# Kernel tuning notes

Hardware: AMD Instinct MI355X
Metric: run time of the kernel (lower is better)

## Reference

```python
import jax, jax.numpy as jnp
import numpy as np

B, D0, D1 = 4096, 128, 128
T, DEPTH, W = 64, 2, 4          # num_tree, depth, width
S = W ** (DEPTH + 1)            # num_state = 64
NODES = sum(W ** l for l in range(DEPTH + 1))  # 21 internal nodes per tree
D = D0 + D1


def setup_inputs() -> dict:
    key = jax.random.key(0)
    ks = jax.random.split(key, 9)
    inp0 = jax.random.normal(ks[0], (B, D0), jnp.float32)
    inp1 = jax.random.normal(ks[1], (B, D1), jnp.float32)
    x2 = jax.random.normal(ks[2], (B,), jnp.float32)
    # ForestLinear: per-tree, per-node linear maps to `width` branch logits
    W_nodes = 0.02 * jax.random.normal(ks[3], (T, NODES, D, W), jnp.float32)
    b_nodes = jnp.zeros((T, NODES, W), jnp.float32)
    # MultiDense([0,1], 1): per-(tree,state) linear probe per input
    W0 = 0.02 * jax.random.normal(ks[4], (T, S, D0), jnp.float32)
    b0 = jnp.zeros((T, S), jnp.float32)
    W1 = 0.02 * jax.random.normal(ks[5], (T, S, D1), jnp.float32)
    b1 = jnp.zeros((T, S), jnp.float32)
    return {"inp0": inp0, "inp1": inp1, "x2": x2,
            "W_nodes": W_nodes, "b_nodes": b_nodes,
            "W0": W0, "b0": b0, "W1": W1, "b1": b1}


def _forest_states(x, W_nodes, b_nodes):
    # x: [B, D] -> leaf-state probabilities [B, T, S]
    logits = jnp.einsum('bd,tndw->btnw', x, W_nodes) + b_nodes  # [B,T,NODES,W]
    probs = jax.nn.softmax(logits, axis=-1)
    p = jnp.ones((x.shape[0], T, 1), probs.dtype)
    off = 0
    for l in range(DEPTH + 1):
        n = W ** l
        pl = probs[:, :, off:off + n, :]                 # [B,T,n,W]
        p = (p[..., None] * pl).reshape(x.shape[0], T, n * W)
        off += n
    return p  # [B, T, S]


def reference(inp0, inp1, x2, W_nodes, b_nodes, W0, b0, W1, b1):
    x_states = _forest_states(jnp.concatenate([inp0, inp1], axis=-1), W_nodes, b_nodes)
    # per-tree/state linear probes; equivalent to tile + MultiDense, no materialized tile
    x_pred = (jnp.einsum('bd,tsd->bts', inp0, W0) + b0
              + jnp.einsum('bd,tsd->bts', inp1, W1) + b1)  # [B,T,S]
    y_pred_logit_parallel = x2[:, None, None] + x_pred
    ave_pred_tree = jnp.sum(x_states * jax.nn.sigmoid(y_pred_logit_parallel), axis=2)  # [B,T]
    ave_pred = jnp.mean(ave_pred_tree, axis=1)  # [B]
    return (y_pred_logit_parallel, ave_pred)
```

## Files before the change

kernel.cpp:

```cpp
#include <hip/hip_runtime.h>

#define B_SZ    4096
#define DD      256
#define T_TREES 64
#define NNODES  21
#define S_LEAF  64
#define M_TILE  128
#define HBYTES  40960
#define WBYTES  (2 * HBYTES)
#define XOFF    ((size_t)T_TREES * WBYTES)
#define QBYTES  20480


typedef __attribute__((ext_vector_type(8))) short  short8;
typedef __attribute__((ext_vector_type(4))) float  f32x4;

#define DPP_ADD(x, ctrl) ((x) + __int_as_float(__builtin_amdgcn_mov_dpp(__float_as_int(x), (ctrl), 0xF, 0xF, true)))
#define DPP_MOV(x, ctrl) __int_as_float(__builtin_amdgcn_mov_dpp(__float_as_int(x), (ctrl), 0xF, 0xF, true))
__device__ __forceinline__ float qsum4(float x) {
    x = DPP_ADD(x, 0xB1);
    x = DPP_ADD(x, 0x4E);
    return x;
}
__device__ __forceinline__ float rsum16(float x) {
    x = DPP_ADD(x, 0xB1);
    x = DPP_ADD(x, 0x4E);
    x = DPP_ADD(x, 0x124);
    x = DPP_ADD(x, 0x128);
    return x;
}

__device__ __forceinline__ unsigned short f2bf(float f) {
    unsigned int u = __float_as_uint(f);
    u += 0x7fffu + ((u >> 16) & 1u);
    return (unsigned short)(u >> 16);
}
__device__ __forceinline__ void gl2lds16(const void* g, void* l) {
    __builtin_amdgcn_global_load_lds(
        (const __attribute__((address_space(1))) unsigned int*)g,
        (__attribute__((address_space(3))) unsigned int*)l, 16, 0, 0);
}
__device__ __host__ __forceinline__ int woffh(int c, int klo) {
    return c * 256 + (((klo ^ c) & 15) << 4);
}
__device__ __host__ __forceinline__ int woffq(int c, int klo) {
    return (c >> 1) * 256 + (((((klo << 1) ^ (c & 14))) | (c & 1)) << 4);
}

__global__ void zero_ave_kernel(float* __restrict__ out1) {
    int i = blockIdx.x * 256 + threadIdx.x;
    if (i < B_SZ) out1[i] = 0.0f;
}

__global__ void prep_weights(const float* __restrict__ Wn, const float* __restrict__ W0,
                             const float* __restrict__ W1, const float* __restrict__ inp0,
                             const float* __restrict__ inp1, char* __restrict__ ws,
                             float* __restrict__ out1) {
    int id = blockIdx.x * 256 + threadIdx.x;
    if (id < 43008) {
        int oct  = id & 31;
        int rest = id >> 5;
        int n    = rest % NNODES;
        int t    = rest / NNODES;
        int h    = oct >> 4, klo = oct & 15;
        const f32x4* src = (const f32x4*)(Wn + (((size_t)t * NNODES + n) * DD + oct * 8) * 4);
        f32x4 v[8];
        #pragma unroll
        for (int j = 0; j < 8; ++j) v[j] = src[j];
        char* base = ws + (size_t)t * WBYTES + h * HBYTES;
        #pragma unroll
        for (int w = 0; w < 4; ++w) {
            int c = n * 4 + w + (n >= 5 ? 12 : 0);
            short8 pack;
            #pragma unroll
            for (int j = 0; j < 8; ++j) pack[j] = (short)f2bf(v[j][w]);
            *(short8*)(base + woffh(c, klo)) = pack;
        }
    } else if (id < 67584) {
        int idx  = id - 43008;
        int kc   = idx & 31;
        int rest = idx >> 5;
        int c    = 20 + rest % 12;
        int t    = rest / 12;
        short8 z = (short8){0,0,0,0,0,0,0,0};
        *(short8*)(ws + (size_t)t * WBYTES + (kc >> 4) * HBYTES + woffh(c, kc & 15)) = z;
    } else if (id < 198656) {
        int idx = id - 67584;
        int kc  = idx & 31;
        int s   = (idx >> 5) & 63;
        int t   = idx >> 11;
        int k0  = kc * 8;
        const float* src = (k0 < 128) ? (W0 + ((size_t)t * S_LEAF + s) * 128 + k0)
                                      : (W1 + ((size_t)t * S_LEAF + s) * 128 + (k0 - 128));
        short8 pack;
        #pragma unroll
        for (int j = 0; j < 8; ++j) pack[j] = (short)f2bf(src[j]);
        *(short8*)(ws + (size_t)t * WBYTES + (kc >> 4) * HBYTES + woffh(96 + s, kc & 15)) = pack;
    } else if (id < 202752) {
        out1[id - 198656] = 0.0f;
    } else if (id < 333824) {
        int idx = id - 202752;
        int oct = idx & 31;
        int r   = idx >> 5;
        const float* src = (oct < 16) ? (inp0 + (size_t)r * 128 + oct * 8)
                                      : (inp1 + (size_t)r * 128 + (oct - 16) * 8);
        f32x4 f0 = *(const f32x4*)src;
        f32x4 f1 = *(const f32x4*)(src + 4);
        short8 pack;
        pack[0]=(short)f2bf(f0[0]); pack[1]=(short)f2bf(f0[1]);
        pack[2]=(short)f2bf(f0[2]); pack[3]=(short)f2bf(f0[3]);
        pack[4]=(short)f2bf(f1[0]); pack[5]=(short)f2bf(f1[1]);
        pack[6]=(short)f2bf(f1[2]); pack[7]=(short)f2bf(f1[3]);
        *(short8*)(ws + XOFF + ((size_t)r * DD + oct * 8) * 2) = pack;
    }
}

__global__ __launch_bounds__(256, 3)
void forest_main(const float* __restrict__ x2,  const float* __restrict__ bn,
                 const float* __restrict__ b0,  const float* __restrict__ b1,
                 const char* __restrict__ wsW,
                 float* __restrict__ out0, float* __restrict__ out1) {
    __shared__ __align__(16) char smem[HBYTES];

    const int tid  = threadIdx.x;
    const int orig = blockIdx.x;
    const int swz  = (orig & 7) * 256 + (orig >> 3);
    const int t    = swz >> 5;
    const int mt   = swz & 31;
    const int m0   = mt * M_TILE;
    const int lane = tid & 63;
    const int wid  = tid >> 6;
    const int ri   = lane & 15;
    const int kg   = lane >> 4;

    const unsigned short* xbf = (const unsigned short*)(wsW + XOFF);
    const char* wbase = wsW + (size_t)t * WBYTES;

    f32x4 acc[2][10];
    #pragma unroll
    for (int sr = 0; sr < 2; ++sr)
        #pragma unroll
        for (int ct = 0; ct < 10; ++ct)
            acc[sr][ct] = (f32x4){0.f, 0.f, 0.f, 0.f};

    const int gr0r = m0 + wid * 32 + ri;
    const int gr1r = gr0r + 16;

    for (int h = 0; h < 2; ++h) {
        {
            const char* src = wbase + h * HBYTES + tid * 16;
            char* dst = smem + tid * 16;
            #pragma unroll
            for (int it = 0; it < 10; ++it)
                gl2lds16(src + it * 4096, dst + it * 4096);
        }
        __syncthreads();

        #pragma unroll
        for (int ks = 0; ks < 4; ++ks) {
            const int kk = h * 4 + ks;
            short8 a0 = *(const short8*)(xbf + (size_t)gr0r * DD + kk * 32 + kg * 8);
            short8 a1 = *(const short8*)(xbf + (size_t)gr1r * DD + kk * 32 + kg * 8);
            const int klo = ks * 4 + kg;
            const int dsB = ri * 256 + (((klo ^ ri) & 15) << 4);
            #pragma unroll
            for (int ct = 0; ct < 10; ++ct) {
                short8 bv = *(const short8*)(smem + dsB + ct * 4096);
                acc[0][ct] = __builtin_amdgcn_mfma_f32_16x16x32_bf16(a0, bv, acc[0][ct], 0, 0, 0);
                acc[1][ct] = __builtin_amdgcn_mfma_f32_16x16x32_bf16(a1, bv, acc[1][ct], 0, 0, 0);
            }
        }
        if (h == 0) __syncthreads();
    }

    const int kgbase = kg * 16;
    #pragma unroll
    for (int sr = 0; sr < 2; ++sr) {
        const int rlBase = wid * 32 + sr * 16 + kg * 4;
        const int gr0 = m0 + rlBase;
        f32x4 x2v = *(const f32x4*)(x2 + gr0);
        float bn0 = bn[t * 84 + ri];
        float bn1 = bn[t * 84 + 16 + (ri & 3)];

        float L1r[4];
        #pragma unroll
        for (int r = 0; r < 4; ++r) {
            float e0 = __expf(acc[sr][0][r] + bn0);
            float p0 = e0 * __builtin_amdgcn_rcpf(qsum4(e0));
            float e1 = __expf(acc[sr][1][r] + bn1);
            float p1 = e1 * __builtin_amdgcn_rcpf(qsum4(e1));
            float pa  = __shfl(p0, kgbase + (ri >> 2));
            float pb0 = DPP_MOV(p0, 0x124);
            float pb1 = DPP_MOV(p1, 0x124);
            L1r[r] = pa * ((ri < 12) ? pb0 : pb1);
        }
        float partial[4] = {0.f, 0.f, 0.f, 0.f};
        #pragma unroll
        for (int ct = 0; ct < 4; ++ct) {
            int s = ct * 16 + ri;
            float bn2 = bn[t * 84 + 20 + s];
            float bb  = b0[t * S_LEAF + s] + b1[t * S_LEAF + s];
            #pragma unroll
            for (int r = 0; r < 4; ++r) {
                float e = __expf(acc[sr][2 + ct][r] + bn2);
                float p2 = e * __builtin_amdgcn_rcpf(qsum4(e));
                float L2 = p2 * __shfl(L1r[r], kgbase + ct * 4 + (ri >> 2));
                float y = acc[sr][6 + ct][r] + x2v[r] + bb;
                out0[((size_t)(gr0 + r) * T_TREES + t) * S_LEAF + s] = y;
                float sg = __builtin_amdgcn_rcpf(1.0f + __expf(-y));
                partial[r] += sg * L2;
            }
        }
        #pragma unroll
        for (int r = 0; r < 4; ++r) {
            float p = rsum16(partial[r]);
            if (ri == 0) atomicAdd(out1 + gr0 + r, p * (1.0f / T_TREES));
        }
    }
}

__device__ __forceinline__ short8 ldAraw(const float* __restrict__ inp0,
                                         const float* __restrict__ inp1,
                                         int gr, int kkidx, int kg) {
    int k0 = kkidx * 32 + kg * 8;
    const float* src = (k0 < 128) ? (inp0 + (size_t)gr * 128 + k0)
                                  : (inp1 + (size_t)gr * 128 + (k0 - 128));
    f32x4 f0 = *(const f32x4*)src;
    f32x4 f1 = *(const f32x4*)(src + 4);
    short8 a;
    a[0]=(short)f2bf(f0[0]); a[1]=(short)f2bf(f0[1]);
    a[2]=(short)f2bf(f0[2]); a[3]=(short)f2bf(f0[3]);
    a[4]=(short)f2bf(f1[0]); a[5]=(short)f2bf(f1[1]);
    a[6]=(short)f2bf(f1[2]); a[7]=(short)f2bf(f1[3]);
    return a;
}

__global__ __launch_bounds__(256, 2)
void forest_fb(const float* __restrict__ inp0, const float* __restrict__ inp1,
               const float* __restrict__ x2,   const float* __restrict__ Wn,
               const float* __restrict__ bn,   const float* __restrict__ W0,
               const float* __restrict__ b0,   const float* __restrict__ W1,
               const float* __restrict__ b1,
               float* __restrict__ out0, float* __restrict__ out1) {
    __shared__ __align__(16) char smem[QBYTES];

    const int tid  = threadIdx.x;
    const int orig = blockIdx.x;
    const int swz  = (orig & 7) * 256 + (orig >> 3);
    const int t    = swz >> 5;
    const int mt   = swz & 31;
    const int m0   = mt * 128;
    const int lane = tid & 63;
    const int wid  = tid >> 6;
    const int ri   = lane & 15;
    const int kg   = lane >> 4;

    f32x4 acc[2][10];
    #pragma unroll
    for (int sr = 0; sr < 2; ++sr)
        #pragma unroll
        for (int ct = 0; ct < 10; ++ct)
            acc[sr][ct] = (f32x4){0.f, 0.f, 0.f, 0.f};

    const int gr0r = m0 + wid * 32 + ri;
    const int gr1r = gr0r + 16;

    int dsb[2];
    #pragma unroll
    for (int kkl = 0; kkl < 2; ++kkl) {
        int klo = kkl * 4 + kg;
        dsb[kkl] = (ri >> 1) * 256 + (((((klo << 1) ^ (ri & 14))) | (ri & 1)) << 4);
    }

    for (int q = 0; q < 4; ++q) {
        #pragma unroll
        for (int it = 0; it < 5; ++it) {
            int idx = tid + it * 256;
            int c   = idx >> 3;
            int klo = idx & 7;
            int k0  = (q * 8 + klo) * 8;
            unsigned short v[8];
            if (c < 20) {
                int n = c >> 2, w = c & 3;
                const float* src = Wn + (((size_t)t * NNODES + n) * DD + k0) * 4 + w;
                #pragma unroll
                for (int j = 0; j < 8; ++j) v[j] = f2bf(src[j * 4]);
            } else if (c < 32) {
                #pragma unroll
                for (int j = 0; j < 8; ++j) v[j] = 0;
            } else if (c < 96) {
                int n = 5 + ((c - 32) >> 2), w = (c - 32) & 3;
                const float* src = Wn + (((size_t)t * NNODES + n) * DD + k0) * 4 + w;
                #pragma unroll
                for (int j = 0; j < 8; ++j) v[j] = f2bf(src[j * 4]);
            } else {
                int s = c - 96;
                const float* src = (k0 < 128) ? (W0 + ((size_t)t * S_LEAF + s) * 128 + k0)
                                              : (W1 + ((size_t)t * S_LEAF + s) * 128 + (k0 - 128));
                #pragma unroll
                for (int j = 0; j < 8; ++j) v[j] = f2bf(src[j]);
            }
            short8 pack;
            #pragma unroll
            for (int j = 0; j < 8; ++j) pack[j] = (short)v[j];
            *(short8*)(smem + woffq(c, klo)) = pack;
        }
        short8 a00 = ldAraw(inp0, inp1, gr0r, 2*q+0, kg);
        short8 a10 = ldAraw(inp0, inp1, gr1r, 2*q+0, kg);
        short8 a01 = ldAraw(inp0, inp1, gr0r, 2*q+1, kg);
        short8 a11 = ldAraw(inp0, inp1, gr1r, 2*q+1, kg);
        __syncthreads();
        #pragma unroll
        for (int ct = 0; ct < 10; ++ct) {
            short8 b0f = *(const short8*)(smem + dsb[0] + ct * 2048);
            acc[0][ct] = __builtin_amdgcn_mfma_f32_16x16x32_bf16(a00, b0f, acc[0][ct], 0, 0, 0);
            acc[1][ct] = __builtin_amdgcn_mfma_f32_16x16x32_bf16(a10, b0f, acc[1][ct], 0, 0, 0);
        }
        #pragma unroll
        for (int ct = 0; ct < 10; ++ct) {
            short8 b1f = *(const short8*)(smem + dsb[1] + ct * 2048);
            acc[0][ct] = __builtin_amdgcn_mfma_f32_16x16x32_bf16(a01, b1f, acc[0][ct], 0, 0, 0);
            acc[1][ct] = __builtin_amdgcn_mfma_f32_16x16x32_bf16(a11, b1f, acc[1][ct], 0, 0, 0);
        }
        if (q < 3) __syncthreads();
    }

    const int kgbase = kg * 16;
    #pragma unroll
    for (int sr = 0; sr < 2; ++sr) {
        const int rlBase = wid * 32 + sr * 16 + kg * 4;
        const int gr0 = m0 + rlBase;
        f32x4 x2v = *(const f32x4*)(x2 + gr0);
        float bn0 = bn[t * 84 + ri];
        float bn1 = bn[t * 84 + 16 + (ri & 3)];
        float L1r[4];
        #pragma unroll
        for (int r = 0; r < 4; ++r) {
            float e0 = __expf(acc[sr][0][r] + bn0);
            float p0 = e0 * __builtin_amdgcn_rcpf(qsum4(e0));
            float e1 = __expf(acc[sr][1][r] + bn1);
            float p1 = e1 * __builtin_amdgcn_rcpf(qsum4(e1));
            float pa  = __shfl(p0, kgbase + (ri >> 2));
            float pb0 = DPP_MOV(p0, 0x124);
            float pb1 = DPP_MOV(p1, 0x124);
            L1r[r] = pa * ((ri < 12) ? pb0 : pb1);
        }
        float partial[4] = {0.f, 0.f, 0.f, 0.f};
        #pragma unroll
        for (int ct = 0; ct < 4; ++ct) {
            int s = ct * 16 + ri;
            float bn2 = bn[t * 84 + 20 + s];
            float bb  = b0[t * S_LEAF + s] + b1[t * S_LEAF + s];
            #pragma unroll
            for (int r = 0; r < 4; ++r) {
                float e = __expf(acc[sr][2 + ct][r] + bn2);
                float p2 = e * __builtin_amdgcn_rcpf(qsum4(e));
                float L2 = p2 * __shfl(L1r[r], kgbase + ct * 4 + (ri >> 2));
                float y = acc[sr][6 + ct][r] + x2v[r] + bb;
                out0[((size_t)(gr0 + r) * T_TREES + t) * S_LEAF + s] = y;
                float sg = __builtin_amdgcn_rcpf(1.0f + __expf(-y));
                partial[r] += sg * L2;
            }
        }
        #pragma unroll
        for (int r = 0; r < 4; ++r) {
            float p = rsum16(partial[r]);
            if (ri == 0) atomicAdd(out1 + gr0 + r, p * (1.0f / T_TREES));
        }
    }
}

extern "C" void kernel_launch(void* const* d_in, const int* in_sizes, int n_in,
                              void* d_out, int out_size, void* d_ws, size_t ws_size,
                              hipStream_t stream) {
    const float* inp0 = (const float*)d_in[0];
    const float* inp1 = (const float*)d_in[1];
    const float* x2   = (const float*)d_in[2];
    const float* Wn   = (const float*)d_in[3];
    const float* bn   = (const float*)d_in[4];
    const float* W0   = (const float*)d_in[5];
    const float* b0   = (const float*)d_in[6];
    const float* W1   = (const float*)d_in[7];
    const float* b1   = (const float*)d_in[8];

    float* out0 = (float*)d_out;
    float* out1 = out0 + (size_t)B_SZ * T_TREES * S_LEAF;

    const size_t need = XOFF + (size_t)B_SZ * DD * 2;
    dim3 grid((B_SZ / M_TILE) * T_TREES);

    if (ws_size >= need) {
        hipLaunchKernelGGL(prep_weights, dim3(1304), dim3(256), 0, stream,
                           Wn, W0, W1, inp0, inp1, (char*)d_ws, out1);
        hipLaunchKernelGGL(forest_main, grid, dim3(256), 0, stream,
                           x2, bn, b0, b1, (const char*)d_ws, out0, out1);
    } else {
        hipLaunchKernelGGL(zero_ave_kernel, dim3((B_SZ + 255) / 256), dim3(256), 0, stream, out1);
        hipLaunchKernelGGL(forest_fb, grid, dim3(256), 0, stream,
                           inp0, inp1, x2, Wn, bn, W0, b0, W1, b1, out0, out1);
    }
}
```

Before: 52.99 us.

## Halve row tile and split column tiles across wave pairs with LDS handoff

Reduces the M tile from 128 to 64 rows, doubling the grid, and splits the 10 output column tiles between two wave groups (5 each), so each wave holds half the accumulators. The tree-probability epilogue is split as well: one wave group computes softmax path probabilities into an LDS table, and the other writes the logits, then combines them with sigmoid after a barrier. Lower register use allows a higher launch-bounds occupancy of 4, at the cost of loading each weight slab twice as often overall, plus an extra barrier and LDS traffic.

Result: slower. 65.57 us (+23.8%).

```diff
diff --git a/kernel.cpp b/kernel.cpp
--- a/kernel.cpp
+++ b/kernel.cpp
@@ -5,7 +5,7 @@
 #define T_TREES 64
 #define NNODES  21
 #define S_LEAF  64
-#define M_TILE  128
+#define M_TILE  64
 #define HBYTES  40960
 #define WBYTES  (2 * HBYTES)
 #define XOFF    ((size_t)T_TREES * WBYTES)
@@ -115,7 +115,7 @@
     }
 }
 
-__global__ __launch_bounds__(256, 3)
+__global__ __launch_bounds__(256, 4)
 void forest_main(const float* __restrict__ x2,  const float* __restrict__ bn,
                  const float* __restrict__ b0,  const float* __restrict__ b1,
                  const char* __restrict__ wsW,
@@ -124,26 +124,28 @@
 
     const int tid  = threadIdx.x;
     const int orig = blockIdx.x;
-    const int swz  = (orig & 7) * 256 + (orig >> 3);
-    const int t    = swz >> 5;
-    const int mt   = swz & 31;
+    const int swz  = (orig & 7) * 512 + (orig >> 3);
+    const int t    = swz >> 6;
+    const int mt   = swz & 63;
     const int m0   = mt * M_TILE;
     const int lane = tid & 63;
     const int wid  = tid >> 6;
+    const int wv   = wid & 1;
+    const int wr   = wid >> 1;
     const int ri   = lane & 15;
     const int kg   = lane >> 4;
 
     const unsigned short* xbf = (const unsigned short*)(wsW + XOFF);
     const char* wbase = wsW + (size_t)t * WBYTES;
 
-    f32x4 acc[2][10];
+    f32x4 acc[2][5];
     #pragma unroll
     for (int sr = 0; sr < 2; ++sr)
         #pragma unroll
-        for (int ct = 0; ct < 10; ++ct)
+        for (int ct = 0; ct < 5; ++ct)
             acc[sr][ct] = (f32x4){0.f, 0.f, 0.f, 0.f};
 
-    const int gr0r = m0 + wid * 32 + ri;
+    const int gr0r = m0 + wr * 32 + ri;
     const int gr1r = gr0r + 16;
 
     for (int h = 0; h < 2; ++h) {
@@ -162,59 +164,110 @@
             short8 a0 = *(const short8*)(xbf + (size_t)gr0r * DD + kk * 32 + kg * 8);
             short8 a1 = *(const short8*)(xbf + (size_t)gr1r * DD + kk * 32 + kg * 8);
             const int klo = ks * 4 + kg;
-            const int dsB = ri * 256 + (((klo ^ ri) & 15) << 4);
-            #pragma unroll
-            for (int ct = 0; ct < 10; ++ct) {
+            const int dsB = wv * 20480 + ri * 256 + (((klo ^ ri) & 15) << 4);
+            #pragma unroll
+            for (int ct = 0; ct < 5; ++ct) {
                 short8 bv = *(const short8*)(smem + dsB + ct * 4096);
                 acc[0][ct] = __builtin_amdgcn_mfma_f32_16x16x32_bf16(a0, bv, acc[0][ct], 0, 0, 0);
                 acc[1][ct] = __builtin_amdgcn_mfma_f32_16x16x32_bf16(a1, bv, acc[1][ct], 0, 0, 0);
             }
         }
-        if (h == 0) __syncthreads();
-    }
-
+        __syncthreads();
+    }
+
+    float* Ltab = (float*)smem;
+    float* L1s  = (float*)smem + 64 * 65;
     const int kgbase = kg * 16;
-    #pragma unroll
-    for (int sr = 0; sr < 2; ++sr) {
-        const int rlBase = wid * 32 + sr * 16 + kg * 4;
-        const int gr0 = m0 + rlBase;
-        f32x4 x2v = *(const f32x4*)(x2 + gr0);
-        float bn0 = bn[t * 84 + ri];
-        float bn1 = bn[t * 84 + 16 + (ri & 3)];
-
-        float L1r[4];
-        #pragma unroll
-        for (int r = 0; r < 4; ++r) {
-            float e0 = __expf(acc[sr][0][r] + bn0);
-            float p0 = e0 * __builtin_amdgcn_rcpf(qsum4(e0));
-            float e1 = __expf(acc[sr][1][r] + bn1);
-            float p1 = e1 * __builtin_amdgcn_rcpf(qsum4(e1));
-            float pa  = __shfl(p0, kgbase + (ri >> 2));
-            float pb0 = DPP_MOV(p0, 0x124);
-            float pb1 = DPP_MOV(p1, 0x124);
-            L1r[r] = pa * ((ri < 12) ? pb0 : pb1);
-        }
-        float partial[4] = {0.f, 0.f, 0.f, 0.f};
-        #pragma unroll
-        for (int ct = 0; ct < 4; ++ct) {
-            int s = ct * 16 + ri;
-            float bn2 = bn[t * 84 + 20 + s];
-            float bb  = b0[t * S_LEAF + s] + b1[t * S_LEAF + s];
+
+    float p48[2][4];
+
+    if (wv == 0) {
+        #pragma unroll
+        for (int sr = 0; sr < 2; ++sr) {
+            const int rowb = wr * 32 + sr * 16 + kg * 4;
+            float bn0 = bn[t * 84 + ri];
+            float bn1 = bn[t * 84 + 16 + (ri & 3)];
+            float L1r[4];
             #pragma unroll
             for (int r = 0; r < 4; ++r) {
-                float e = __expf(acc[sr][2 + ct][r] + bn2);
-                float p2 = e * __builtin_amdgcn_rcpf(qsum4(e));
-                float L2 = p2 * __shfl(L1r[r], kgbase + ct * 4 + (ri >> 2));
-                float y = acc[sr][6 + ct][r] + x2v[r] + bb;
-                out0[((size_t)(gr0 + r) * T_TREES + t) * S_LEAF + s] = y;
-                float sg = __builtin_amdgcn_rcpf(1.0f + __expf(-y));
-                partial[r] += sg * L2;
-            }
-        }
-        #pragma unroll
-        for (int r = 0; r < 4; ++r) {
-            float p = rsum16(partial[r]);
-            if (ri == 0) atomicAdd(out1 + gr0 + r, p * (1.0f / T_TREES));
+                float e0 = __expf(acc[sr][0][r] + bn0);
+                float p0 = e0 * __builtin_amdgcn_rcpf(qsum4(e0));
+                float e1 = __expf(acc[sr][1][r] + bn1);
+                float p1 = e1 * __builtin_amdgcn_rcpf(qsum4(e1));
+                float pa  = __shfl(p0, kgbase + (ri >> 2));
+                float pb0 = DPP_MOV(p0, 0x124);
+                float pb1 = DPP_MOV(p1, 0x124);
+                L1r[r] = pa * ((ri < 12) ? pb0 : pb1);
+                if (ri >= 12) L1s[(rowb + r) * 4 + (ri - 12)] = L1r[r];
+            }
+            #pragma unroll
+            for (int ct = 2; ct < 5; ++ct) {
+                int s = (ct - 2) * 16 + ri;
+                float bn2 = bn[t * 84 + 20 + s];
+                #pragma unroll
+                for (int r = 0; r < 4; ++r) {
+                    float e = __expf(acc[sr][ct][r] + bn2);
+                    float p2 = e * __builtin_amdgcn_rcpf(qsum4(e));
+                    float L2 = p2 * __shfl(L1r[r], kgbase + (ct - 2) * 4 + (ri >> 2));
+                    Ltab[(rowb + r) * 65 + s] = L2;
+                }
+            }
+        }
+    } else {
+        float bn2 = bn[t * 84 + 68 + ri];
+        #pragma unroll
+        for (int sr = 0; sr < 2; ++sr)
+            #pragma unroll
+            for (int r = 0; r < 4; ++r) {
+                float e = __expf(acc[sr][0][r] + bn2);
+                p48[sr][r] = e * __builtin_amdgcn_rcpf(qsum4(e));
+            }
+        #pragma unroll
+        for (int sr = 0; sr < 2; ++sr) {
+            const int gr0 = m0 + wr * 32 + sr * 16 + kg * 4;
+            f32x4 x2v = *(const f32x4*)(x2 + gr0);
+            #pragma unroll
+            for (int ct = 1; ct < 5; ++ct) {
+                int s = (ct - 1) * 16 + ri;
+                float bb = b0[t * S_LEAF + s] + b1[t * S_LEAF + s];
+                #pragma unroll
+                for (int r = 0; r < 4; ++r) {
+                    float y = acc[sr][ct][r] + x2v[r] + bb;
+                    out0[((size_t)(gr0 + r) * T_TREES + t) * S_LEAF + s] = y;
+                }
+            }
+        }
+    }
+    __syncthreads();
+
+    if (wv == 1) {
+        #pragma unroll
+        for (int sr = 0; sr < 2; ++sr) {
+            const int rowb = wr * 32 + sr * 16 + kg * 4;
+            const int gr0 = m0 + rowb;
+            f32x4 x2v = *(const f32x4*)(x2 + gr0);
+            float L2_48[4];
+            #pragma unroll
+            for (int r = 0; r < 4; ++r)
+                L2_48[r] = p48[sr][r] * L1s[(rowb + r) * 4 + (ri >> 2)];
+            float partial[4] = {0.f, 0.f, 0.f, 0.f};
+            #pragma unroll
+            for (int ct = 1; ct < 5; ++ct) {
+                int s = (ct - 1) * 16 + ri;
+                float bb = b0[t * S_LEAF + s] + b1[t * S_LEAF + s];
+                #pragma unroll
+                for (int r = 0; r < 4; ++r) {
+                    float y = acc[sr][ct][r] + x2v[r] + bb;
+                    float sg = __builtin_amdgcn_rcpf(1.0f + __expf(-y));
+                    float L2 = (ct < 4) ? Ltab[(rowb + r) * 65 + s] : L2_48[r];
+                    partial[r] += sg * L2;
+                }
+            }
+            #pragma unroll
+            for (int r = 0; r < 4; ++r) {
+                float p = rsum16(partial[r]);
+                if (ri == 0) atomicAdd(out1 + gr0 + r, p * (1.0f / T_TREES));
+            }
         }
     }
 }
@@ -387,16 +440,15 @@
     float* out1 = out0 + (size_t)B_SZ * T_TREES * S_LEAF;
 
     const size_t need = XOFF + (size_t)B_SZ * DD * 2;
-    dim3 grid((B_SZ / M_TILE) * T_TREES);
 
     if (ws_size >= need) {
         hipLaunchKernelGGL(prep_weights, dim3(1304), dim3(256), 0, stream,
                            Wn, W0, W1, inp0, inp1, (char*)d_ws, out1);
-        hipLaunchKernelGGL(forest_main, grid, dim3(256), 0, stream,
+        hipLaunchKernelGGL(forest_main, dim3((B_SZ / M_TILE) * T_TREES), dim3(256), 0, stream,
                            x2, bn, b0, b1, (const char*)d_ws, out0, out1);
     } else {
         hipLaunchKernelGGL(zero_ave_kernel, dim3((B_SZ + 255) / 256), dim3(256), 0, stream, out1);
-        hipLaunchKernelGGL(forest_fb, grid, dim3(256), 0, stream,
+        hipLaunchKernelGGL(forest_fb, dim3((B_SZ / 128) * T_TREES), dim3(256), 0, stream,
                            inp0, inp1, x2, Wn, bn, W0, b0, W1, b1, out0, out1);
     }
 }
```

## Load full per-tree weights into LDS once and loop over four row tiles

Applied to the files above, without the earlier changes.

Each block now stages the whole 80KB weight slab for a tree into shared memory in a single pass. It then processes four 128-row tiles (512 rows) against those weights, instead of reloading weights in two halves for every 128-row tile. This cuts weight traffic and removes the mid-loop barrier. In exchange the grid is 4x smaller (512 blocks), LDS use doubles, and launch bounds drop to 2 blocks per CU, which lowers occupancy and latency hiding.

Result: slower. 121.3 us (+129.0%).

```diff
diff --git a/kernel.cpp b/kernel.cpp
--- a/kernel.cpp
+++ b/kernel.cpp
@@ -5,7 +5,7 @@
 #define T_TREES 64
 #define NNODES  21
 #define S_LEAF  64
-#define M_TILE  128
+#define M_SUP   512
 #define HBYTES  40960
 #define WBYTES  (2 * HBYTES)
 #define XOFF    ((size_t)T_TREES * WBYTES)
@@ -115,19 +115,19 @@
     }
 }
 
-__global__ __launch_bounds__(256, 3)
+__global__ __launch_bounds__(256, 2)
 void forest_main(const float* __restrict__ x2,  const float* __restrict__ bn,
                  const float* __restrict__ b0,  const float* __restrict__ b1,
                  const char* __restrict__ wsW,
                  float* __restrict__ out0, float* __restrict__ out1) {
-    __shared__ __align__(16) char smem[HBYTES];
+    __shared__ __align__(16) char smem[WBYTES];
 
     const int tid  = threadIdx.x;
     const int orig = blockIdx.x;
-    const int swz  = (orig & 7) * 256 + (orig >> 3);
-    const int t    = swz >> 5;
-    const int mt   = swz & 31;
-    const int m0   = mt * M_TILE;
+    const int swz  = (orig & 7) * 64 + (orig >> 3);
+    const int t    = swz >> 3;
+    const int st   = swz & 7;
+    const int m0   = st * M_SUP;
     const int lane = tid & 63;
     const int wid  = tid >> 6;
     const int ri   = lane & 15;
@@ -136,33 +136,35 @@
     const unsigned short* xbf = (const unsigned short*)(wsW + XOFF);
     const char* wbase = wsW + (size_t)t * WBYTES;
 
-    f32x4 acc[2][10];
-    #pragma unroll
-    for (int sr = 0; sr < 2; ++sr)
-        #pragma unroll
-        for (int ct = 0; ct < 10; ++ct)
-            acc[sr][ct] = (f32x4){0.f, 0.f, 0.f, 0.f};
-
-    const int gr0r = m0 + wid * 32 + ri;
-    const int gr1r = gr0r + 16;
-
-    for (int h = 0; h < 2; ++h) {
-        {
-            const char* src = wbase + h * HBYTES + tid * 16;
-            char* dst = smem + tid * 16;
-            #pragma unroll
-            for (int it = 0; it < 10; ++it)
-                gl2lds16(src + it * 4096, dst + it * 4096);
-        }
-        __syncthreads();
-
-        #pragma unroll
-        for (int ks = 0; ks < 4; ++ks) {
-            const int kk = h * 4 + ks;
+    {
+        const char* src = wbase + tid * 16;
+        char* dst = smem + tid * 16;
+        #pragma unroll
+        for (int it = 0; it < 20; ++it)
+            gl2lds16(src + it * 4096, dst + it * 4096);
+    }
+    __syncthreads();
+
+    const int kgbase = kg * 16;
+
+    for (int rt = 0; rt < 4; ++rt) {
+        const int r0 = m0 + rt * 128;
+        const int gr0r = r0 + wid * 32 + ri;
+        const int gr1r = gr0r + 16;
+
+        f32x4 acc[2][10];
+        #pragma unroll
+        for (int sr = 0; sr < 2; ++sr)
+            #pragma unroll
+            for (int ct = 0; ct < 10; ++ct)
+                acc[sr][ct] = (f32x4){0.f, 0.f, 0.f, 0.f};
+
+        #pragma unroll
+        for (int kk = 0; kk < 8; ++kk) {
             short8 a0 = *(const short8*)(xbf + (size_t)gr0r * DD + kk * 32 + kg * 8);
             short8 a1 = *(const short8*)(xbf + (size_t)gr1r * DD + kk * 32 + kg * 8);
-            const int klo = ks * 4 + kg;
-            const int dsB = ri * 256 + (((klo ^ ri) & 15) << 4);
+            const int klo = (kk & 3) * 4 + kg;
+            const int dsB = (kk >> 2) * HBYTES + ri * 256 + (((klo ^ ri) & 15) << 4);
             #pragma unroll
             for (int ct = 0; ct < 10; ++ct) {
                 short8 bv = *(const short8*)(smem + dsB + ct * 4096);
@@ -170,51 +172,48 @@
                 acc[1][ct] = __builtin_amdgcn_mfma_f32_16x16x32_bf16(a1, bv, acc[1][ct], 0, 0, 0);
             }
         }
-        if (h == 0) __syncthreads();
-    }
-
-    const int kgbase = kg * 16;
-    #pragma unroll
-    for (int sr = 0; sr < 2; ++sr) {
-        const int rlBase = wid * 32 + sr * 16 + kg * 4;
-        const int gr0 = m0 + rlBase;
-        f32x4 x2v = *(const f32x4*)(x2 + gr0);
-        float bn0 = bn[t * 84 + ri];
-        float bn1 = bn[t * 84 + 16 + (ri & 3)];
-
-        float L1r[4];
-        #pragma unroll
-        for (int r = 0; r < 4; ++r) {
-            float e0 = __expf(acc[sr][0][r] + bn0);
-            float p0 = e0 * __builtin_amdgcn_rcpf(qsum4(e0));
-            float e1 = __expf(acc[sr][1][r] + bn1);
-            float p1 = e1 * __builtin_amdgcn_rcpf(qsum4(e1));
-            float pa  = __shfl(p0, kgbase + (ri >> 2));
-            float pb0 = DPP_MOV(p0, 0x124);
-            float pb1 = DPP_MOV(p1, 0x124);
-            L1r[r] = pa * ((ri < 12) ? pb0 : pb1);
-        }
-        float partial[4] = {0.f, 0.f, 0.f, 0.f};
-        #pragma unroll
-        for (int ct = 0; ct < 4; ++ct) {
-            int s = ct * 16 + ri;
-            float bn2 = bn[t * 84 + 20 + s];
-            float bb  = b0[t * S_LEAF + s] + b1[t * S_LEAF + s];
+
+        #pragma unroll
+        for (int sr = 0; sr < 2; ++sr) {
+            const int gr0 = r0 + wid * 32 + sr * 16 + kg * 4;
+            f32x4 x2v = *(const f32x4*)(x2 + gr0);
+            float bn0 = bn[t * 84 + ri];
+            float bn1 = bn[t * 84 + 16 + (ri & 3)];
+
+            float L1r[4];
             #pragma unroll
             for (int r = 0; r < 4; ++r) {
-                float e = __expf(acc[sr][2 + ct][r] + bn2);
-                float p2 = e * __builtin_amdgcn_rcpf(qsum4(e));
-                float L2 = p2 * __shfl(L1r[r], kgbase + ct * 4 + (ri >> 2));
-                float y = acc[sr][6 + ct][r] + x2v[r] + bb;
-                out0[((size_t)(gr0 + r) * T_TREES + t) * S_LEAF + s] = y;
-                float sg = __builtin_amdgcn_rcpf(1.0f + __expf(-y));
-                partial[r] += sg * L2;
-            }
-        }
-        #pragma unroll
-        for (int r = 0; r < 4; ++r) {
-            float p = rsum16(partial[r]);
-            if (ri == 0) atomicAdd(out1 + gr0 + r, p * (1.0f / T_TREES));
+                float e0 = __expf(acc[sr][0][r] + bn0);
+                float p0 = e0 * __builtin_amdgcn_rcpf(qsum4(e0));
+                float e1 = __expf(acc[sr][1][r] + bn1);
+                float p1 = e1 * __builtin_amdgcn_rcpf(qsum4(e1));
+                float pa  = __shfl(p0, kgbase + (ri >> 2));
+                float pb0 = DPP_MOV(p0, 0x124);
+                float pb1 = DPP_MOV(p1, 0x124);
+                L1r[r] = pa * ((ri < 12) ? pb0 : pb1);
+            }
+            float partial[4] = {0.f, 0.f, 0.f, 0.f};
+            #pragma unroll
+            for (int ct = 0; ct < 4; ++ct) {
+                int s = ct * 16 + ri;
+                float bn2 = bn[t * 84 + 20 + s];
+                float bb  = b0[t * S_LEAF + s] + b1[t * S_LEAF + s];
+                #pragma unroll
+                for (int r = 0; r < 4; ++r) {
+                    float e = __expf(acc[sr][2 + ct][r] + bn2);
+                    float p2 = e * __builtin_amdgcn_rcpf(qsum4(e));
+                    float L2 = p2 * __shfl(L1r[r], kgbase + ct * 4 + (ri >> 2));
+                    float y = acc[sr][6 + ct][r] + x2v[r] + bb;
+                    out0[((size_t)(gr0 + r) * T_TREES + t) * S_LEAF + s] = y;
+                    float sg = __builtin_amdgcn_rcpf(1.0f + __expf(-y));
+                    partial[r] += sg * L2;
+                }
+            }
+            #pragma unroll
+            for (int r = 0; r < 4; ++r) {
+                float p = rsum16(partial[r]);
+                if (ri == 0) atomicAdd(out1 + gr0 + r, p * (1.0f / T_TREES));
+            }
         }
     }
 }
@@ -387,16 +386,15 @@
     float* out1 = out0 + (size_t)B_SZ * T_TREES * S_LEAF;
 
     const size_t need = XOFF + (size_t)B_SZ * DD * 2;
-    dim3 grid((B_SZ / M_TILE) * T_TREES);
 
     if (ws_size >= need) {
         hipLaunchKernelGGL(prep_weights, dim3(1304), dim3(256), 0, stream,
                            Wn, W0, W1, inp0, inp1, (char*)d_ws, out1);
-        hipLaunchKernelGGL(forest_main, grid, dim3(256), 0, stream,
+        hipLaunchKernelGGL(forest_main, dim3((B_SZ / M_SUP) * T_TREES), dim3(256), 0, stream,
                            x2, bn, b0, b1, (const char*)d_ws, out0, out1);
     } else {
         hipLaunchKernelGGL(zero_ave_kernel, dim3((B_SZ + 255) / 256), dim3(256), 0, stream, out1);
-        hipLaunchKernelGGL(forest_fb, grid, dim3(256), 0, stream,
+        hipLaunchKernelGGL(forest_fb, dim3((B_SZ / 128) * T_TREES), dim3(256), 0, stream,
                            inp0, inp1, x2, Wn, bn, W0, b0, W1, b1, out0, out1);
     }
 }
```

## Use 512-thread blocks with one 16-row subtile per wave and prefetch A

Applied to the files above, without the earlier changes.

The block grows from 4 to 8 waves, and each wave now computes a single 16-row subtile instead of two, which halves the accumulator registers. The launch bound rises to 512 threads with 4 blocks per CU, aiming for more resident waves to hide latency. The shared-memory weight staging is spread across twice as many threads, and the next A fragment is register-prefetched one k-step ahead. In exchange, each B fragment read from LDS now feeds only one MFMA instead of two, which doubles LDS traffic per FLOP.

Measured after the change: 48.24 us, median of 2. -8.9%, faster.

```diff
diff --git a/kernel.cpp b/kernel.cpp
--- a/kernel.cpp
+++ b/kernel.cpp
@@ -115,7 +115,7 @@
     }
 }
 
-__global__ __launch_bounds__(256, 3)
+__global__ __launch_bounds__(512, 4)
 void forest_main(const float* __restrict__ x2,  const float* __restrict__ bn,
                  const float* __restrict__ b0,  const float* __restrict__ b1,
                  const char* __restrict__ wsW,
@@ -136,47 +136,45 @@
     const unsigned short* xbf = (const unsigned short*)(wsW + XOFF);
     const char* wbase = wsW + (size_t)t * WBYTES;
 
-    f32x4 acc[2][10];
+    f32x4 acc[10];
     #pragma unroll
-    for (int sr = 0; sr < 2; ++sr)
-        #pragma unroll
-        for (int ct = 0; ct < 10; ++ct)
-            acc[sr][ct] = (f32x4){0.f, 0.f, 0.f, 0.f};
-
-    const int gr0r = m0 + wid * 32 + ri;
-    const int gr1r = gr0r + 16;
+    for (int ct = 0; ct < 10; ++ct)
+        acc[ct] = (f32x4){0.f, 0.f, 0.f, 0.f};
+
+    const int grr = m0 + wid * 16 + ri;
+    const unsigned short* aBase = xbf + (size_t)grr * DD + kg * 8;
 
     for (int h = 0; h < 2; ++h) {
         {
             const char* src = wbase + h * HBYTES + tid * 16;
             char* dst = smem + tid * 16;
             #pragma unroll
-            for (int it = 0; it < 10; ++it)
-                gl2lds16(src + it * 4096, dst + it * 4096);
-        }
+            for (int it = 0; it < 5; ++it)
+                gl2lds16(src + it * 8192, dst + it * 8192);
+        }
+        short8 a = *(const short8*)(aBase + (h * 4) * 32);
         __syncthreads();
 
         #pragma unroll
         for (int ks = 0; ks < 4; ++ks) {
-            const int kk = h * 4 + ks;
-            short8 a0 = *(const short8*)(xbf + (size_t)gr0r * DD + kk * 32 + kg * 8);
-            short8 a1 = *(const short8*)(xbf + (size_t)gr1r * DD + kk * 32 + kg * 8);
+            short8 an;
+            if (ks < 3)
+                an = *(const short8*)(aBase + (h * 4 + ks + 1) * 32);
             const int klo = ks * 4 + kg;
             const int dsB = ri * 256 + (((klo ^ ri) & 15) << 4);
             #pragma unroll
             for (int ct = 0; ct < 10; ++ct) {
                 short8 bv = *(const short8*)(smem + dsB + ct * 4096);
-                acc[0][ct] = __builtin_amdgcn_mfma_f32_16x16x32_bf16(a0, bv, acc[0][ct], 0, 0, 0);
-                acc[1][ct] = __builtin_amdgcn_mfma_f32_16x16x32_bf16(a1, bv, acc[1][ct], 0, 0, 0);
+                acc[ct] = __builtin_amdgcn_mfma_f32_16x16x32_bf16(a, bv, acc[ct], 0, 0, 0);
             }
+            a = an;
         }
         if (h == 0) __syncthreads();
     }
 
     const int kgbase = kg * 16;
-    #pragma unroll
-    for (int sr = 0; sr < 2; ++sr) {
-        const int rlBase = wid * 32 + sr * 16 + kg * 4;
+    {
+        const int rlBase = wid * 16 + kg * 4;
         const int gr0 = m0 + rlBase;
         f32x4 x2v = *(const f32x4*)(x2 + gr0);
         float bn0 = bn[t * 84 + ri];
@@ -185,9 +183,9 @@
         float L1r[4];
         #pragma unroll
         for (int r = 0; r < 4; ++r) {
-            float e0 = __expf(acc[sr][0][r] + bn0);
+            float e0 = __expf(acc[0][r] + bn0);
             float p0 = e0 * __builtin_amdgcn_rcpf(qsum4(e0));
-            float e1 = __expf(acc[sr][1][r] + bn1);
+            float e1 = __expf(acc[1][r] + bn1);
             float p1 = e1 * __builtin_amdgcn_rcpf(qsum4(e1));
             float pa  = __shfl(p0, kgbase + (ri >> 2));
             float pb0 = DPP_MOV(p0, 0x124);
@@ -202,10 +200,10 @@
             float bb  = b0[t * S_LEAF + s] + b1[t * S_LEAF + s];
             #pragma unroll
             for (int r = 0; r < 4; ++r) {
-                float e = __expf(acc[sr][2 + ct][r] + bn2);
+                float e = __expf(acc[2 + ct][r] + bn2);
                 float p2 = e * __builtin_amdgcn_rcpf(qsum4(e));
                 float L2 = p2 * __shfl(L1r[r], kgbase + ct * 4 + (ri >> 2));
-                float y = acc[sr][6 + ct][r] + x2v[r] + bb;
+                float y = acc[6 + ct][r] + x2v[r] + bb;
                 out0[((size_t)(gr0 + r) * T_TREES + t) * S_LEAF + s] = y;
                 float sg = __builtin_amdgcn_rcpf(1.0f + __expf(-y));
                 partial[r] += sg * L2;
@@ -392,7 +390,7 @@
     if (ws_size >= need) {
         hipLaunchKernelGGL(prep_weights, dim3(1304), dim3(256), 0, stream,
                            Wn, W0, W1, inp0, inp1, (char*)d_ws, out1);
-        hipLaunchKernelGGL(forest_main, grid, dim3(256), 0, stream,
+        hipLaunchKernelGGL(forest_main, grid, dim3(512), 0, stream,
                            x2, bn, b0, b1, (const char*)d_ws, out0, out1);
     } else {
         hipLaunchKernelGGL(zero_ave_kernel, dim3((B_SZ + 255) / 256), dim3(256), 0, stream, out1);
```
